# Kernel optimization log

Measured on AMD Instinct MI355X. Metric: run time of the kernel, lower is better.

Reference implementation:

```python
import jax, jax.numpy as jnp
import numpy as np

C = 1024
H = 16
HS = C // H
HID = 4096
A_MIX = 0.7
B_MIX = 0.3
EPS = 1e-5


def layernorm(x, w, b):
    mu = jnp.mean(x, axis=-1, keepdims=True)
    var = jnp.mean(jnp.square(x - mu), axis=-1, keepdims=True)
    return (x - mu) * jax.lax.rsqrt(var + EPS) * w + b


def setup_inputs() -> dict:
    key = jax.random.key(0)
    ks = jax.random.split(key, 12)
    B, N = 4, 1024
    s = 1.0 / np.sqrt(C)
    sh = 1.0 / np.sqrt(HID)
    return {
        "x": jax.random.normal(ks[0], (B, N, C), jnp.float32),
        "Query": jax.random.normal(ks[1], (B, H, N, HS), jnp.float32),
        "Key": jax.random.normal(ks[2], (B, H, N, HS), jnp.float32),
        "Value": jax.random.normal(ks[3], (B, H, N, HS), jnp.float32),
        "ln_w": jnp.ones((C,), jnp.float32),
        "ln_b": jnp.zeros((C,), jnp.float32),
        "qk_w": jax.random.normal(ks[4], (2 * C, C), jnp.float32) * s,
        "qk_b": jnp.zeros((2 * C,), jnp.float32),
        "v_w": jax.random.normal(ks[5], (C, C), jnp.float32) * s,
        "v_b": jnp.zeros((C,), jnp.float32),
        "out_w": jax.random.normal(ks[6], (C, C), jnp.float32) * s,
        "out_b": jnp.zeros((C,), jnp.float32),
        "mlp_w1": jax.random.normal(ks[7], (HID, C), jnp.float32) * s,
        "mlp_b1": jnp.zeros((HID,), jnp.float32),
        "mlp_w2": jax.random.normal(ks[8], (C, HID), jnp.float32) * sh,
        "mlp_b2": jnp.zeros((C,), jnp.float32),
    }


def reference(x, Query, Key, Value, ln_w, ln_b, qk_w, qk_b, v_w, v_b,
              out_w, out_b, mlp_w1, mlp_b1, mlp_w2, mlp_b2):
    B, N, _ = x.shape
    x1 = x
    xn = layernorm(x, ln_w, ln_b)
    # qk projection -> view (B,N,H,HS,2), permute -> (2,B,H,N,HS)
    qk = (xn @ qk_w.T + qk_b).reshape(B, N, H, HS, 2)
    Q = jnp.transpose(qk[..., 0], (0, 2, 1, 3))  # (B,H,N,HS)
    K = jnp.transpose(qk[..., 1], (0, 2, 1, 3))
    V = jnp.transpose((xn @ v_w.T + v_b).reshape(B, N, H, HS), (0, 2, 1, 3))
    Query = A_MIX * Q + B_MIX * Query
    Key = A_MIX * K + B_MIX * Key
    Value = B_MIX * Value + A_MIX * V
    attn = jnp.einsum('bhqd,bhkd->bhqk', Query, Key) / np.sqrt(HS)
    attn = jax.nn.softmax(attn, axis=-1)  # dropout = identity in eval
    o = jnp.einsum('bhqk,bhkd->bhqd', attn, Value)
    o = jnp.transpose(o, (0, 2, 1, 3)).reshape(B, N, C)
    o = o @ out_w.T + out_b
    x = x1 + o
    x2 = x
    xn2 = layernorm(x, ln_w, ln_b)  # same layernorm params reused
    h = jax.nn.gelu(xn2 @ mlp_w1.T + mlp_b1, approximate=False)
    m = h @ mlp_w2.T + mlp_b2
    return (m + x2, Query, Key, Value)
```

## Files before the change

### kernel.cpp

```cpp
#include <hip/hip_runtime.h>

using bf16x8 = __attribute__((ext_vector_type(8))) __bf16;
using f32x4  = __attribute__((ext_vector_type(4))) float;

#define AS1(p) (const __attribute__((address_space(1))) void*)(p)
#define AS3(p) (__attribute__((address_space(3))) void*)(p)

__device__ __forceinline__ unsigned short f2bf(float f) {
    unsigned int u = __float_as_uint(f);
    unsigned int r = (u + 0x7FFFu + ((u >> 16) & 1u)) >> 16;
    return (unsigned short)r;
}
__device__ __forceinline__ float bf2f(unsigned short u) {
    return __uint_as_float((unsigned int)u << 16);
}
__device__ __forceinline__ float gelu_fast(float x) {
    const float a = 1.5957691f * (x + 0.044715f * x * x * x);
    return x / (1.0f + __expf(-a));
}

__global__ __launch_bounds__(256) void cvt_kernel(const float* __restrict__ in,
                                                  unsigned short* __restrict__ out,
                                                  int n) {
    int i = (blockIdx.x * 256 + threadIdx.x) * 4;
    if (i < n) {
        float4 v = *(const float4*)(in + i);
        ushort4 o = make_ushort4(f2bf(v.x), f2bf(v.y), f2bf(v.z), f2bf(v.w));
        *(ushort4*)(out + i) = o;
    }
}

__global__ __launch_bounds__(256) void ln_kernel(const float* __restrict__ in,
                                                 const float* __restrict__ w,
                                                 const float* __restrict__ b,
                                                 unsigned short* __restrict__ out) {
    const int row = blockIdx.x;
    const int tid = threadIdx.x;
    const float4 v = *(const float4*)(in + (size_t)row * 1024 + tid * 4);
    float s  = v.x + v.y + v.z + v.w;
    float ss = v.x * v.x + v.y * v.y + v.z * v.z + v.w * v.w;
    #pragma unroll
    for (int m = 1; m < 64; m <<= 1) {
        s  += __shfl_xor(s, m, 64);
        ss += __shfl_xor(ss, m, 64);
    }
    __shared__ float red[8];
    if ((tid & 63) == 0) { red[(tid >> 6) * 2] = s; red[(tid >> 6) * 2 + 1] = ss; }
    __syncthreads();
    s  = red[0] + red[2] + red[4] + red[6];
    ss = red[1] + red[3] + red[5] + red[7];
    const float mu  = s * (1.0f / 1024.0f);
    const float var = ss * (1.0f / 1024.0f) - mu * mu;
    const float rstd = rsqrtf(var + 1e-5f);
    const float4 wv = *(const float4*)(w + tid * 4);
    const float4 bv = *(const float4*)(b + tid * 4);
    ushort4 o;
    o.x = f2bf((v.x - mu) * rstd * wv.x + bv.x);
    o.y = f2bf((v.y - mu) * rstd * wv.y + bv.y);
    o.z = f2bf((v.z - mu) * rstd * wv.z + bv.z);
    o.w = f2bf((v.w - mu) * rstd * wv.w + bv.w);
    *(ushort4*)(out + (size_t)row * 1024 + tid * 4) = o;
}

template <int EPI>
__global__ __launch_bounds__(256, 2)
void gemm_bt(const unsigned short* __restrict__ A,
             const unsigned short* __restrict__ W,
             const float* __restrict__ bias,
             int M, int N, int K,
             const float* __restrict__ e0, const float* __restrict__ e1,
             float* __restrict__ o0, float* __restrict__ o1,
             unsigned short* __restrict__ u0, unsigned short* __restrict__ u1) {
    __shared__ unsigned short As[128 * 128];
    __shared__ unsigned short Bs[128 * 128];
    const int tid  = threadIdx.x;
    const int wave = tid >> 6, lane = tid & 63;
    const int wr = wave >> 1, wc = wave & 1;
    const int q15 = lane & 15, g = lane >> 4;

    const int gx = gridDim.x;
    const int nwg = gx * gridDim.y;
    int flat = blockIdx.y * gx + blockIdx.x;
    flat = (flat & 7) * (nwg >> 3) + (flat >> 3);
    const int gm0 = (flat / gx) * 128, gn0 = (flat % gx) * 128;

    f32x4 acc[4][4] = {};

    const int lrow4 = lane >> 4;
    const int lslot = lane & 15;
    const int rswz  = q15 << 4;

    for (int k0 = 0; k0 < K; k0 += 128) {
        #pragma unroll
        for (int i = 0; i < 8; ++i) {
            const int row  = wave * 32 + i * 4 + lrow4;
            const int selm = (lslot ^ (row & 15)) << 3;
            __builtin_amdgcn_global_load_lds(AS1(A + (size_t)(gm0 + row) * K + k0 + selm),
                                             AS3((char*)As + wave * 8192 + i * 1024), 16, 0, 0);
            __builtin_amdgcn_global_load_lds(AS1(W + (size_t)(gn0 + row) * K + k0 + selm),
                                             AS3((char*)Bs + wave * 8192 + i * 1024), 16, 0, 0);
        }
        __syncthreads();
        #pragma unroll
        for (int kk = 0; kk < 4; ++kk) {
            bf16x8 af[4], bfr[4];
            #pragma unroll
            for (int m = 0; m < 4; ++m)
                af[m] = *(const bf16x8*)((char*)As + (wr * 64 + m * 16 + q15) * 256 +
                                         ((kk * 64 + g * 16) ^ rswz));
            #pragma unroll
            for (int n = 0; n < 4; ++n)
                bfr[n] = *(const bf16x8*)((char*)Bs + (wc * 64 + n * 16 + q15) * 256 +
                                          ((kk * 64 + g * 16) ^ rswz));
            #pragma unroll
            for (int m = 0; m < 4; ++m)
                #pragma unroll
                for (int n = 0; n < 4; ++n)
                    acc[m][n] = __builtin_amdgcn_mfma_f32_16x16x32_bf16(af[m], bfr[n], acc[m][n], 0, 0, 0);
        }
        __syncthreads();
    }

    #pragma unroll
    for (int m = 0; m < 4; ++m)
    #pragma unroll
    for (int n = 0; n < 4; ++n)
    #pragma unroll
    for (int j = 0; j < 4; ++j) {
        const int r = gm0 + wr * 64 + m * 16 + g * 4 + j;
        const int c = gn0 + wc * 64 + n * 16 + q15;
        const float val = acc[m][n][j] + bias[c];
        if constexpr (EPI == 0) {
            const int bb = r >> 10, nn = r & 1023;
            const int h = c >> 7, hs = (c >> 1) & 63, isk = c & 1;
            const size_t idx = (((size_t)(bb * 16 + h)) * 1024 + nn) * 64 + hs;
            if (!isk) { const float mx = 0.7f * val + 0.3f * e0[idx]; o0[idx] = mx; u0[idx] = f2bf(mx); }
            else      { const float mx = 0.7f * val + 0.3f * e1[idx]; o1[idx] = mx; u1[idx] = f2bf(mx); }
        } else if constexpr (EPI == 1) {
            const int bb = r >> 10, nn = r & 1023;
            const int h = c >> 6, hs = c & 63;
            const size_t idx = (((size_t)(bb * 16 + h)) * 1024 + nn) * 64 + hs;
            const float mx = 0.7f * val + 0.3f * e0[idx];
            o0[idx] = mx;
            u0[(((size_t)(bb * 16 + h)) * 64 + hs) * 1024 + nn] = f2bf(mx);
        } else {
            const size_t idx = (size_t)r * N + c;
            o0[idx] = val + e0[idx];
        }
    }
}

__global__ __launch_bounds__(512, 1)
void gemm_big_gelu(const unsigned short* __restrict__ A,
                   const unsigned short* __restrict__ W,
                   const float* __restrict__ bias,
                   int M, int N, int K,
                   unsigned short* __restrict__ u0) {
    __shared__ unsigned short Ls[3][2][256 * 32];
    const int tid  = threadIdx.x;
    const int wave = tid >> 6, lane = tid & 63;
    const int wr = wave >> 2, wc = wave & 3;
    const int q15 = lane & 15, g = lane >> 4;

    const int gx = gridDim.x;
    const int nwg = gx * gridDim.y;
    int flat = blockIdx.y * gx + blockIdx.x;
    flat = (flat & 7) * (nwg >> 3) + (flat >> 3);
    const int gm0 = (flat / gx) * 256, gn0 = (flat % gx) * 256;

    f32x4 acc[8][4] = {};

    const int srow  = tid >> 2;
    const int sslot = (tid & 3) ^ ((srow >> 1) & 3);
    const int selm  = sslot << 3;

    #define STAGEH(kt, p, rb)                                                        \
        {                                                                            \
            const unsigned short* src_ = ((p) < 2) ? A : W;                          \
            const int gbase_ = ((p) < 2) ? gm0 : gn0;                                \
            const int row_ = ((p) & 1) * 128 + srow;                                 \
            __builtin_amdgcn_global_load_lds(                                        \
                AS1(src_ + (size_t)(gbase_ + row_) * K + (kt) * 32 + selm),          \
                AS3((char*)Ls[rb][(p) >> 1] + ((p) & 1) * 8192 + tid * 16),          \
                16, 0, 0);                                                           \
        }

    const int nt = K >> 5;
    #pragma unroll
    for (int p = 0; p < 4; ++p) STAGEH(0, p, 0);
    #pragma unroll
    for (int p = 0; p < 4; ++p) STAGEH(1, p, 1);

    int rb = 0;
    for (int t = 0; t < nt; ++t) {
        if (t >= nt - 1) { asm volatile("s_waitcnt vmcnt(0)" ::: "memory"); }
        else             { asm volatile("s_waitcnt vmcnt(4)" ::: "memory"); }
        asm volatile("s_barrier" ::: "memory");
        const int rb2 = (rb >= 1) ? rb - 1 : rb + 2;
        const char* Ab = (const char*)Ls[rb][0];
        const char* Bb = (const char*)Ls[rb][1];
        #pragma unroll
        for (int p = 0; p < 4; ++p) {
            if (t + 2 < nt) STAGEH(t + 2, p, rb2);
            const int mh = p >> 1, nh = p & 1;
            bf16x8 af[4], bf[2];
            #pragma unroll
            for (int mm = 0; mm < 4; ++mm) {
                const int row = wr * 128 + mh * 64 + mm * 16 + q15;
                af[mm] = *(const bf16x8*)(Ab + row * 64 + ((g ^ ((row >> 1) & 3)) << 4));
            }
            #pragma unroll
            for (int nn = 0; nn < 2; ++nn) {
                const int row = wc * 64 + nh * 32 + nn * 16 + q15;
                bf[nn] = *(const bf16x8*)(Bb + row * 64 + ((g ^ ((row >> 1) & 3)) << 4));
            }
            __builtin_amdgcn_s_setprio(1);
            #pragma unroll
            for (int mm = 0; mm < 4; ++mm)
                #pragma unroll
                for (int nn = 0; nn < 2; ++nn)
                    acc[mh * 4 + mm][nh * 2 + nn] = __builtin_amdgcn_mfma_f32_16x16x32_bf16(
                        af[mm], bf[nn], acc[mh * 4 + mm][nh * 2 + nn], 0, 0, 0);
            __builtin_amdgcn_s_setprio(0);
        }
        rb = (rb == 2) ? 0 : rb + 1;
    }
    #undef STAGEH

    #pragma unroll
    for (int m = 0; m < 8; ++m)
    #pragma unroll
    for (int n = 0; n < 4; ++n)
    #pragma unroll
    for (int j = 0; j < 4; ++j) {
        const int r = gm0 + wr * 128 + m * 16 + g * 4 + j;
        const int c = gn0 + wc * 64 + n * 16 + q15;
        const float val = acc[m][n][j] + bias[c];
        u0[(size_t)r * N + c] = f2bf(gelu_fast(val));
    }
}

__global__ __launch_bounds__(256, 6)
void attn_kernel(const unsigned short* __restrict__ Qb,
                 const unsigned short* __restrict__ Kb,
                 const unsigned short* __restrict__ Vt,
                 unsigned short* __restrict__ Op,
                 float* __restrict__ Mws,
                 float* __restrict__ Lws) {
    const int bh = blockIdx.y;
    const int z  = blockIdx.z;
    const int tid = threadIdx.x, wave = tid >> 6, lane = tid & 63;
    const int qbase = blockIdx.x * 64 + wave * 16;
    const int q15 = lane & 15, g = lane >> 4;

    const unsigned short* Qh = Qb + (size_t)bh * 1024 * 64;
    const unsigned short* Kh = Kb + (size_t)bh * 1024 * 64;
    const unsigned short* Vh = Vt + (size_t)bh * 64 * 1024;

    __shared__ alignas(128) unsigned short Ks[64 * 64];
    __shared__ alignas(128) unsigned short Vs[64 * 64];
    __shared__ alignas(128) unsigned short Ps[4][1024];
    char* const Pb = (char*)Ps[wave] + q15 * 128;
    const int swz = (q15 & 7) << 4;

    const int srow8 = lane >> 3;
    const int selm  = (((lane & 7) ^ srow8) << 3);

    bf16x8 aq[2];
    aq[0] = *(const bf16x8*)&Qh[(size_t)(qbase + q15) * 64 + 0  + g * 8];
    aq[1] = *(const bf16x8*)&Qh[(size_t)(qbase + q15) * 64 + 32 + g * 8];

    f32x4 o[4] = {};
    float mrow = -1e30f, lrow = 0.f;

    const int t0 = z * 8;
    for (int t = t0; t < t0 + 8; ++t) {
        const int kb = t * 64;
        #pragma unroll
        for (int i = 0; i < 2; ++i) {
            const int r = wave * 16 + i * 8 + srow8;
            __builtin_amdgcn_global_load_lds(AS1(Kh + (size_t)(kb + r) * 64 + selm),
                                             AS3((char*)Ks + wave * 2048 + i * 1024), 16, 0, 0);
            __builtin_amdgcn_global_load_lds(AS1(Vh + (size_t)r * 1024 + kb + selm),
                                             AS3((char*)Vs + wave * 2048 + i * 1024), 16, 0, 0);
        }
        __syncthreads();

        f32x4 s[4] = {};
        #pragma unroll
        for (int kt = 0; kt < 4; ++kt) {
            #pragma unroll
            for (int kk = 0; kk < 2; ++kk) {
                const bf16x8 bk = *(const bf16x8*)((char*)Ks + (kt * 16 + q15) * 128 +
                                                   ((kk * 64 + g * 16) ^ swz));
                s[kt] = __builtin_amdgcn_mfma_f32_16x16x32_bf16(bk, aq[kk], s[kt], 0, 0, 0);
            }
        }
        float pm = -1e30f;
        #pragma unroll
        for (int kt = 0; kt < 4; ++kt) {
            s[kt] *= 0.125f;
            pm = fmaxf(pm, fmaxf(fmaxf(s[kt][0], s[kt][1]), fmaxf(s[kt][2], s[kt][3])));
        }
        pm = fmaxf(pm, __shfl_xor(pm, 16, 64));
        pm = fmaxf(pm, __shfl_xor(pm, 32, 64));
        const float mnew = fmaxf(mrow, pm);
        const float alpha = __expf(mrow - mnew);
        mrow = mnew;

        float rs = 0.f;
        #pragma unroll
        for (int kt = 0; kt < 4; ++kt) {
            const float p0 = __expf(s[kt][0] - mnew);
            const float p1 = __expf(s[kt][1] - mnew);
            const float p2 = __expf(s[kt][2] - mnew);
            const float p3 = __expf(s[kt][3] - mnew);
            rs += (p0 + p1) + (p2 + p3);
            uint2 pk;
            pk.x = (unsigned int)f2bf(p0) | ((unsigned int)f2bf(p1) << 16);
            pk.y = (unsigned int)f2bf(p2) | ((unsigned int)f2bf(p3) << 16);
            *(uint2*)(Pb + (((kt * 32 + g * 8) ^ swz))) = pk;
        }
        rs += __shfl_xor(rs, 16, 64);
        rs += __shfl_xor(rs, 32, 64);
        lrow = lrow * alpha + rs;

        float af[4];
        #pragma unroll
        for (int j = 0; j < 4; ++j) af[j] = __shfl(alpha, g * 4 + j, 64);
        #pragma unroll
        for (int dt = 0; dt < 4; ++dt)
            #pragma unroll
            for (int j = 0; j < 4; ++j) o[dt][j] *= af[j];

        #pragma unroll
        for (int Bb = 0; Bb < 2; ++Bb) {
            const bf16x8 pa = *(const bf16x8*)(Pb + (((Bb * 64 + g * 16) ^ swz)));
            #pragma unroll
            for (int dt = 0; dt < 4; ++dt) {
                const bf16x8 vb = *(const bf16x8*)((char*)Vs + (dt * 16 + q15) * 128 +
                                                   ((Bb * 64 + g * 16) ^ swz));
                o[dt] = __builtin_amdgcn_mfma_f32_16x16x32_bf16(pa, vb, o[dt], 0, 0, 0);
            }
        }
        __syncthreads();
    }

    #pragma unroll
    for (int dt = 0; dt < 4; ++dt)
        #pragma unroll
        for (int j = 0; j < 4; ++j) {
            const int q = qbase + g * 4 + j;
            Op[(((size_t)z * 64 + bh) * 1024 + q) * 64 + dt * 16 + q15] = f2bf(o[dt][j]);
        }
    if (g == 0) {
        const size_t mi = ((size_t)z * 64 + bh) * 1024 + qbase + q15;
        Mws[mi] = mrow;
        Lws[mi] = lrow;
    }
}

__global__ __launch_bounds__(256)
void attn_combine(const unsigned short* __restrict__ Op,
                  const float* __restrict__ Mws,
                  const float* __restrict__ Lws,
                  unsigned short* __restrict__ Ob) {
    const int e4 = blockIdx.x * 256 + threadIdx.x;
    const int d0 = (e4 & 15) * 4;
    const int q  = (e4 >> 4) & 1023;
    const int bh = e4 >> 14;
    const size_t base0 = (((size_t)bh) * 1024 + q) * 64 + d0;
    const size_t base1 = (((size_t)(64 + bh)) * 1024 + q) * 64 + d0;
    const ushort4 a = *(const ushort4*)&Op[base0];
    const ushort4 c = *(const ushort4*)&Op[base1];
    const size_t mi0 = (size_t)bh * 1024 + q;
    const size_t mi1 = mi0 + 64 * 1024;
    const float m0 = Mws[mi0], m1 = Mws[mi1];
    const float l0 = Lws[mi0], l1 = Lws[mi1];
    const float m  = fmaxf(m0, m1);
    const float w0 = __expf(m0 - m), w1 = __expf(m1 - m);
    const float inv = 1.0f / (l0 * w0 + l1 * w1);
    ushort4 r;
    r.x = f2bf((bf2f(a.x) * w0 + bf2f(c.x) * w1) * inv);
    r.y = f2bf((bf2f(a.y) * w0 + bf2f(c.y) * w1) * inv);
    r.z = f2bf((bf2f(a.z) * w0 + bf2f(c.z) * w1) * inv);
    r.w = f2bf((bf2f(a.w) * w0 + bf2f(c.w) * w1) * inv);
    const int b = bh >> 4, h = bh & 15;
    *(ushort4*)&Ob[((size_t)(b * 1024 + q)) * 1024 + h * 64 + d0] = r;
}

extern "C" void kernel_launch(void* const* d_in, const int* in_sizes, int n_in,
                              void* d_out, int out_size, void* d_ws, size_t ws_size,
                              hipStream_t stream) {
    (void)in_sizes; (void)n_in; (void)out_size; (void)ws_size;
    const float* x     = (const float*)d_in[0];
    const float* Qin   = (const float*)d_in[1];
    const float* Kin   = (const float*)d_in[2];
    const float* Vin   = (const float*)d_in[3];
    const float* ln_w  = (const float*)d_in[4];
    const float* ln_b  = (const float*)d_in[5];
    const float* qk_w  = (const float*)d_in[6];
    const float* qk_b  = (const float*)d_in[7];
    const float* v_w   = (const float*)d_in[8];
    const float* v_b   = (const float*)d_in[9];
    const float* out_w = (const float*)d_in[10];
    const float* out_b = (const float*)d_in[11];
    const float* w1    = (const float*)d_in[12];
    const float* b1    = (const float*)d_in[13];
    const float* w2    = (const float*)d_in[14];
    const float* b2    = (const float*)d_in[15];

    const size_t FOUR_M = (size_t)4 * 1024 * 1024;
    float* out0 = (float*)d_out;
    float* Qout = out0 + FOUR_M;
    float* Kout = Qout + FOUR_M;
    float* Vout = Kout + FOUR_M;

    char* ws = (char*)d_ws;
    const size_t MB = 1024 * 1024;
    unsigned short* xn   = (unsigned short*)(ws + 0);
    unsigned short* qkwb = (unsigned short*)(ws + 8 * MB);
    unsigned short* vwb  = (unsigned short*)(ws + 12 * MB);
    unsigned short* owb  = (unsigned short*)(ws + 14 * MB);
    unsigned short* w1b  = (unsigned short*)(ws + 16 * MB);
    unsigned short* w2b  = (unsigned short*)(ws + 24 * MB);
    unsigned short* Qbuf = (unsigned short*)(ws + 32 * MB);
    unsigned short* Kbuf = (unsigned short*)(ws + 40 * MB);
    unsigned short* Vtb  = (unsigned short*)(ws + 48 * MB);
    unsigned short* atto = (unsigned short*)(ws + 56 * MB);
    unsigned short* hbuf = (unsigned short*)(ws + 32 * MB);
    float* y1 = (float*)(ws + 64 * MB);
    unsigned short* Oprt = (unsigned short*)(ws + 64 * MB);
    float* Mws = (float*)(ws + 8 * MB);
    float* Lws = (float*)(ws + 8 * MB + 512 * 1024);

    cvt_kernel<<<2048, 256, 0, stream>>>(qk_w, qkwb, 2048 * 1024);
    cvt_kernel<<<1024, 256, 0, stream>>>(v_w,  vwb,  1024 * 1024);
    cvt_kernel<<<1024, 256, 0, stream>>>(out_w, owb, 1024 * 1024);
    cvt_kernel<<<4096, 256, 0, stream>>>(w1, w1b, 4096 * 1024);
    cvt_kernel<<<4096, 256, 0, stream>>>(w2, w2b, 4096 * 1024);

    ln_kernel<<<4096, 256, 0, stream>>>(x, ln_w, ln_b, xn);

    {
        dim3 g(2048 / 128, 4096 / 128);
        gemm_bt<0><<<g, 256, 0, stream>>>(xn, qkwb, qk_b, 4096, 2048, 1024,
                                          Qin, Kin, Qout, Kout, Qbuf, Kbuf);
    }
    {
        dim3 g(1024 / 128, 4096 / 128);
        gemm_bt<1><<<g, 256, 0, stream>>>(xn, vwb, v_b, 4096, 1024, 1024,
                                          Vin, nullptr, Vout, nullptr, Vtb, nullptr);
    }
    {
        dim3 g(16, 64, 2);
        attn_kernel<<<g, 256, 0, stream>>>(Qbuf, Kbuf, Vtb, Oprt, Mws, Lws);
        attn_combine<<<4096, 256, 0, stream>>>(Oprt, Mws, Lws, atto);
    }
    {
        dim3 g(1024 / 128, 4096 / 128);
        gemm_bt<2><<<g, 256, 0, stream>>>(atto, owb, out_b, 4096, 1024, 1024,
                                          x, nullptr, y1, nullptr, nullptr, nullptr);
    }
    ln_kernel<<<4096, 256, 0, stream>>>(y1, ln_w, ln_b, xn);
    {
        dim3 g(4096 / 256, 4096 / 256);
        gemm_big_gelu<<<g, 512, 0, stream>>>(xn, w1b, b1, 4096, 4096, 1024, hbuf);
    }
    {
        dim3 g(1024 / 128, 4096 / 128);
        gemm_bt<2><<<g, 256, 0, stream>>>(hbuf, w2b, b2, 4096, 1024, 4096,
                                          y1, nullptr, out0, nullptr, nullptr, nullptr);
    }
}
```

Measured before the change: 259.8 us.

## Split-K the second MLP GEMM using the large-tile kernel with bf16 partials

Generalizes the 256x256 large-tile GEMM with a K-split offset and an epilogue template. The down-projection then runs as a 4-way split-K on it instead of the 128x128 kernel with a long K loop. Slice 0 writes bias plus residual in fp32, the other slices write bf16 partials, and a new combine kernel adds them. This aims for better per-block MFMA efficiency and shorter serial K loops, at the cost of extra partial traffic, an additional launch and bf16 rounding of the partial sums.

```diff
diff --git a/kernel.cpp b/kernel.cpp
--- a/kernel.cpp
+++ b/kernel.cpp
@@ -150,12 +150,15 @@
     }
 }
 
+template <int EPI>
 __global__ __launch_bounds__(512, 1)
-void gemm_big_gelu(const unsigned short* __restrict__ A,
-                   const unsigned short* __restrict__ W,
-                   const float* __restrict__ bias,
-                   int M, int N, int K,
-                   unsigned short* __restrict__ u0) {
+void gemm_big(const unsigned short* __restrict__ A,
+              const unsigned short* __restrict__ W,
+              const float* __restrict__ bias,
+              int M, int N, int lda, int Kc,
+              const float* __restrict__ e0,
+              float* __restrict__ o0,
+              unsigned short* __restrict__ u0) {
     __shared__ unsigned short Ls[3][2][256 * 32];
     const int tid  = threadIdx.x;
     const int wave = tid >> 6, lane = tid & 63;
@@ -167,6 +170,7 @@
     int flat = blockIdx.y * gx + blockIdx.x;
     flat = (flat & 7) * (nwg >> 3) + (flat >> 3);
     const int gm0 = (flat / gx) * 256, gn0 = (flat % gx) * 256;
+    const int k0base = blockIdx.z * Kc;
 
     f32x4 acc[8][4] = {};
 
@@ -180,12 +184,12 @@
             const int gbase_ = ((p) < 2) ? gm0 : gn0;                                \
             const int row_ = ((p) & 1) * 128 + srow;                                 \
             __builtin_amdgcn_global_load_lds(                                        \
-                AS1(src_ + (size_t)(gbase_ + row_) * K + (kt) * 32 + selm),          \
+                AS1(src_ + (size_t)(gbase_ + row_) * lda + k0base + (kt) * 32 + selm), \
                 AS3((char*)Ls[rb][(p) >> 1] + ((p) & 1) * 8192 + tid * 16),          \
                 16, 0, 0);                                                           \
         }
 
-    const int nt = K >> 5;
+    const int nt = Kc >> 5;
     #pragma unroll
     for (int p = 0; p < 4; ++p) STAGEH(0, p, 0);
     #pragma unroll
@@ -235,8 +239,36 @@
     for (int j = 0; j < 4; ++j) {
         const int r = gm0 + wr * 128 + m * 16 + g * 4 + j;
         const int c = gn0 + wc * 64 + n * 16 + q15;
-        const float val = acc[m][n][j] + bias[c];
-        u0[(size_t)r * N + c] = f2bf(gelu_fast(val));
+        if constexpr (EPI == 0) {
+            const float val = acc[m][n][j] + bias[c];
+            u0[(size_t)r * N + c] = f2bf(gelu_fast(val));
+        } else {
+            if (blockIdx.z == 0) {
+                const float val = acc[m][n][j] + bias[c];
+                const size_t idx = (size_t)r * N + c;
+                o0[idx] = val + e0[idx];
+            } else {
+                u0[((size_t)(blockIdx.z - 1) * M + r) * N + c] = f2bf(acc[m][n][j]);
+            }
+        }
+    }
+}
+
+__global__ __launch_bounds__(256)
+void mlp2_combine(float* __restrict__ out0,
+                  const unsigned short* __restrict__ Pp,
+                  int total) {
+    const int i = (blockIdx.x * 256 + threadIdx.x) * 4;
+    if (i < total) {
+        float4 v = *(float4*)(out0 + i);
+        const ushort4 p1 = *(const ushort4*)&Pp[i];
+        const ushort4 p2 = *(const ushort4*)&Pp[(size_t)total + i];
+        const ushort4 p3 = *(const ushort4*)&Pp[(size_t)2 * total + i];
+        v.x += bf2f(p1.x) + bf2f(p2.x) + bf2f(p3.x);
+        v.y += bf2f(p1.y) + bf2f(p2.y) + bf2f(p3.y);
+        v.z += bf2f(p1.z) + bf2f(p2.z) + bf2f(p3.z);
+        v.w += bf2f(p1.w) + bf2f(p2.w) + bf2f(p3.w);
+        *(float4*)(out0 + i) = v;
     }
 }
 
@@ -433,6 +465,7 @@
     unsigned short* Oprt = (unsigned short*)(ws + 64 * MB);
     float* Mws = (float*)(ws + 8 * MB);
     float* Lws = (float*)(ws + 8 * MB + 512 * 1024);
+    unsigned short* Pmlp = (unsigned short*)(ws + 0);
 
     cvt_kernel<<<2048, 256, 0, stream>>>(qk_w, qkwb, 2048 * 1024);
     cvt_kernel<<<1024, 256, 0, stream>>>(v_w,  vwb,  1024 * 1024);
@@ -464,12 +497,14 @@
     }
     ln_kernel<<<4096, 256, 0, stream>>>(y1, ln_w, ln_b, xn);
     {
-        dim3 g(4096 / 256, 4096 / 256);
-        gemm_big_gelu<<<g, 512, 0, stream>>>(xn, w1b, b1, 4096, 4096, 1024, hbuf);
+        dim3 g(4096 / 256, 4096 / 256, 1);
+        gemm_big<0><<<g, 512, 0, stream>>>(xn, w1b, b1, 4096, 4096, 1024, 1024,
+                                           nullptr, nullptr, hbuf);
     }
     {
-        dim3 g(1024 / 128, 4096 / 128);
-        gemm_bt<2><<<g, 256, 0, stream>>>(hbuf, w2b, b2, 4096, 1024, 4096,
-                                          y1, nullptr, out0, nullptr, nullptr, nullptr);
-    }
-}
+        dim3 g(1024 / 256, 4096 / 256, 4);
+        gemm_big<1><<<g, 512, 0, stream>>>(hbuf, w2b, b2, 4096, 1024, 4096, 1024,
+                                           y1, out0, Pmlp);
+        mlp2_combine<<<4096, 256, 0, stream>>>(out0, Pmlp, 4 * 1024 * 1024);
+    }
+}
```

Measured after the change: 281.6 us. +8.4%, slower.

## Retile MLP-up GELU GEMM to 256x128 tiles with 4 waves, 2 blocks/CU

Applied to the files above, without the earlier changes.

Changes the big GELU GEMM from 256x256 tiles on 512 threads (1 block per CU) to 256x128 tiles on 256 threads with a 2-blocks-per-CU occupancy hint. The grid doubles to 512 blocks. Each wave now computes a 128x64 sub-tile, and the prefetch of the next K-tile is split into three chunks interleaved with the LDS fragment loads and MFMA groups. The goal is better CU load balance and overlap between blocks, with the async loads spread through the compute. In exchange, B operand reuse per loaded A tile is lower, and two resident blocks compete for LDS and registers.

```diff
diff --git a/kernel.cpp b/kernel.cpp
--- a/kernel.cpp
+++ b/kernel.cpp
@@ -150,79 +150,92 @@
     }
 }
 
-__global__ __launch_bounds__(512, 1)
+__global__ __launch_bounds__(256, 2)
 void gemm_big_gelu(const unsigned short* __restrict__ A,
                    const unsigned short* __restrict__ W,
                    const float* __restrict__ bias,
                    int M, int N, int K,
                    unsigned short* __restrict__ u0) {
-    __shared__ unsigned short Ls[3][2][256 * 32];
+    __shared__ unsigned short Ls[3][12288];
     const int tid  = threadIdx.x;
     const int wave = tid >> 6, lane = tid & 63;
-    const int wr = wave >> 2, wc = wave & 3;
+    const int wr = wave >> 1, wc = wave & 1;
     const int q15 = lane & 15, g = lane >> 4;
 
     const int gx = gridDim.x;
     const int nwg = gx * gridDim.y;
     int flat = blockIdx.y * gx + blockIdx.x;
     flat = (flat & 7) * (nwg >> 3) + (flat >> 3);
-    const int gm0 = (flat / gx) * 256, gn0 = (flat % gx) * 256;
+    const int gm0 = (flat / gx) * 256, gn0 = (flat % gx) * 128;
 
     f32x4 acc[8][4] = {};
 
-    const int srow  = tid >> 2;
-    const int sslot = (tid & 3) ^ ((srow >> 1) & 3);
-    const int selm  = sslot << 3;
-
-    #define STAGEH(kt, p, rb)                                                        \
+    const int rloc0 = wave * 32 + (lane >> 2);
+    const int rloc1 = rloc0 + 16;
+    const int slot  = lane & 3;
+    const int selm0 = (slot ^ ((rloc0 >> 1) & 3)) << 3;
+    const int selm1 = (slot ^ ((rloc1 >> 1) & 3)) << 3;
+
+    #define STAGEH(kt, half, rb)                                                     \
         {                                                                            \
-            const unsigned short* src_ = ((p) < 2) ? A : W;                          \
-            const int gbase_ = ((p) < 2) ? gm0 : gn0;                                \
-            const int row_ = ((p) & 1) * 128 + srow;                                 \
+            const unsigned short* src_ = ((half) < 2) ? A : W;                       \
+            const int gb_ = ((half) == 0) ? gm0 : (((half) == 1) ? gm0 + 128 : gn0); \
+            const int lb_ = ((half) < 2) ? (half) * 8192 : 16384;                    \
             __builtin_amdgcn_global_load_lds(                                        \
-                AS1(src_ + (size_t)(gbase_ + row_) * K + (kt) * 32 + selm),          \
-                AS3((char*)Ls[rb][(p) >> 1] + ((p) & 1) * 8192 + tid * 16),          \
-                16, 0, 0);                                                           \
+                AS1(src_ + (size_t)(gb_ + rloc0) * K + (kt) * 32 + selm0),           \
+                AS3((char*)Ls[rb] + lb_ + wave * 2048), 16, 0, 0);                   \
+            __builtin_amdgcn_global_load_lds(                                        \
+                AS1(src_ + (size_t)(gb_ + rloc1) * K + (kt) * 32 + selm1),           \
+                AS3((char*)Ls[rb] + lb_ + wave * 2048 + 1024), 16, 0, 0);            \
         }
 
     const int nt = K >> 5;
-    #pragma unroll
-    for (int p = 0; p < 4; ++p) STAGEH(0, p, 0);
-    #pragma unroll
-    for (int p = 0; p < 4; ++p) STAGEH(1, p, 1);
+    STAGEH(0, 0, 0); STAGEH(0, 1, 0); STAGEH(0, 2, 0);
+    STAGEH(1, 0, 1); STAGEH(1, 1, 1); STAGEH(1, 2, 1);
 
     int rb = 0;
     for (int t = 0; t < nt; ++t) {
         if (t >= nt - 1) { asm volatile("s_waitcnt vmcnt(0)" ::: "memory"); }
-        else             { asm volatile("s_waitcnt vmcnt(4)" ::: "memory"); }
+        else             { asm volatile("s_waitcnt vmcnt(6)" ::: "memory"); }
         asm volatile("s_barrier" ::: "memory");
         const int rb2 = (rb >= 1) ? rb - 1 : rb + 2;
-        const char* Ab = (const char*)Ls[rb][0];
-        const char* Bb = (const char*)Ls[rb][1];
-        #pragma unroll
-        for (int p = 0; p < 4; ++p) {
-            if (t + 2 < nt) STAGEH(t + 2, p, rb2);
-            const int mh = p >> 1, nh = p & 1;
-            bf16x8 af[4], bf[2];
-            #pragma unroll
-            for (int mm = 0; mm < 4; ++mm) {
-                const int row = wr * 128 + mh * 64 + mm * 16 + q15;
-                af[mm] = *(const bf16x8*)(Ab + row * 64 + ((g ^ ((row >> 1) & 3)) << 4));
-            }
-            #pragma unroll
-            for (int nn = 0; nn < 2; ++nn) {
-                const int row = wc * 64 + nh * 32 + nn * 16 + q15;
-                bf[nn] = *(const bf16x8*)(Bb + row * 64 + ((g ^ ((row >> 1) & 3)) << 4));
-            }
-            __builtin_amdgcn_s_setprio(1);
-            #pragma unroll
-            for (int mm = 0; mm < 4; ++mm)
-                #pragma unroll
-                for (int nn = 0; nn < 2; ++nn)
-                    acc[mh * 4 + mm][nh * 2 + nn] = __builtin_amdgcn_mfma_f32_16x16x32_bf16(
-                        af[mm], bf[nn], acc[mh * 4 + mm][nh * 2 + nn], 0, 0, 0);
-            __builtin_amdgcn_s_setprio(0);
-        }
+        const char* Ab = (const char*)Ls[rb];
+        const char* Bb = (const char*)Ls[rb] + 16384;
+        const bool pf = (t + 2 < nt);
+
+        if (pf) STAGEH(t + 2, 0, rb2);
+        bf16x8 bf[4], af[4];
+        #pragma unroll
+        for (int n = 0; n < 4; ++n) {
+            const int row = wc * 64 + n * 16 + q15;
+            bf[n] = *(const bf16x8*)(Bb + row * 64 + ((g ^ ((row >> 1) & 3)) << 4));
+        }
+        #pragma unroll
+        for (int m = 0; m < 4; ++m) {
+            const int row = wr * 128 + m * 16 + q15;
+            af[m] = *(const bf16x8*)(Ab + row * 64 + ((g ^ ((row >> 1) & 3)) << 4));
+        }
+        if (pf) STAGEH(t + 2, 1, rb2);
+        __builtin_amdgcn_s_setprio(1);
+        #pragma unroll
+        for (int m = 0; m < 4; ++m)
+            #pragma unroll
+            for (int n = 0; n < 4; ++n)
+                acc[m][n] = __builtin_amdgcn_mfma_f32_16x16x32_bf16(af[m], bf[n], acc[m][n], 0, 0, 0);
+        __builtin_amdgcn_s_setprio(0);
+        if (pf) STAGEH(t + 2, 2, rb2);
+        #pragma unroll
+        for (int m = 0; m < 4; ++m) {
+            const int row = wr * 128 + 64 + m * 16 + q15;
+            af[m] = *(const bf16x8*)(Ab + row * 64 + ((g ^ ((row >> 1) & 3)) << 4));
+        }
+        __builtin_amdgcn_s_setprio(1);
+        #pragma unroll
+        for (int m = 0; m < 4; ++m)
+            #pragma unroll
+            for (int n = 0; n < 4; ++n)
+                acc[4 + m][n] = __builtin_amdgcn_mfma_f32_16x16x32_bf16(af[m], bf[n], acc[4 + m][n], 0, 0, 0);
+        __builtin_amdgcn_s_setprio(0);
         rb = (rb == 2) ? 0 : rb + 1;
     }
     #undef STAGEH
@@ -233,7 +246,7 @@
     for (int n = 0; n < 4; ++n)
     #pragma unroll
     for (int j = 0; j < 4; ++j) {
-        const int r = gm0 + wr * 128 + m * 16 + g * 4 + j;
+        const int r = gm0 + wr * 128 + (m >> 2) * 64 + (m & 3) * 16 + g * 4 + j;
         const int c = gn0 + wc * 64 + n * 16 + q15;
         const float val = acc[m][n][j] + bias[c];
         u0[(size_t)r * N + c] = f2bf(gelu_fast(val));
@@ -464,8 +477,8 @@
     }
     ln_kernel<<<4096, 256, 0, stream>>>(y1, ln_w, ln_b, xn);
     {
-        dim3 g(4096 / 256, 4096 / 256);
-        gemm_big_gelu<<<g, 512, 0, stream>>>(xn, w1b, b1, 4096, 4096, 1024, hbuf);
+        dim3 g(4096 / 128, 4096 / 256);
+        gemm_big_gelu<<<g, 256, 0, stream>>>(xn, w1b, b1, 4096, 4096, 1024, hbuf);
     }
     {
         dim3 g(1024 / 128, 4096 / 128);
```

After: 270.0 us. +3.9%, slower.
